# Kernel tuning notes

Measured on AMD Instinct MI355X. Metric: run time of the kernel, lower is better.

The kernel has to match this reference:

```python
import jax, jax.numpy as jnp
import numpy as np

B, N = 16, 131072
C_MID, C_OUT = 128, 16


def setup_inputs() -> dict:
    key = jax.random.key(0)
    k1, k2, k3, k4 = jax.random.split(key, 4)
    # points in roughly [-0.5, 0.5] so cube indexing covers the grids
    x = jax.random.uniform(k1, (B, N, 3), dtype=jnp.float32) - 0.5
    W1 = jax.random.normal(k2, (C_MID, 3), dtype=jnp.float32) * 0.1
    b1 = jnp.zeros((C_MID,), jnp.float32)
    W2 = jax.random.normal(k3, (C_OUT, C_MID), dtype=jnp.float32) * 0.1
    b2 = jnp.zeros((C_OUT,), jnp.float32)
    # fixed per-batch permutations (deterministic stand-in for torch.randperm)
    perm = jnp.stack([jax.random.permutation(jax.random.fold_in(k4, i), N)
                      for i in range(B)]).astype(jnp.int32)
    return {"x": x, "W1": W1, "b1": b1, "W2": W2, "b2": b2, "perm": perm}


def point_to_cell(pts, feat, W, H, D):
    # pts float [B,N,3] already clamped to [0, dim-1]; cast like torch LongTensor
    idx = pts.astype(jnp.int32)
    flat = (idx[..., 0] * H + idx[..., 1]) * D + idx[..., 2]  # [B,N]
    Bb, Nn, C = feat.shape

    def scatter_one(fi, fe):
        grid = jnp.zeros((W * H * D, C), feat.dtype)
        return grid.at[fi].set(fe)

    cell = jax.vmap(scatter_one)(flat, feat)           # [B, WHD, C]
    return cell.transpose(0, 2, 1).reshape(Bb, C, W, H, D)


def reference(x, W1, b1, W2, b2, perm):
    # PointNetfeatLocal: 1x1 Conv1d stack == per-point MLP 3 -> 128 -> 16
    h = jnp.maximum(jnp.einsum('bnc,hc->bnh', x, W1) + b1, 0.0)
    feat = jnp.einsum('bnh,oh->bno', h, W2) + b2       # [B,N,16]
    # shuffle_points_feat: per-batch permutation gather
    xs = jnp.take_along_axis(x, perm[..., None], axis=1)
    fs = jnp.take_along_axis(feat, perm[..., None], axis=1)
    # batch_grid_pooling32 / 64
    cube32 = jnp.clip(xs * 32.0 + 16.5, 0.0, 31.0)
    cube64 = jnp.clip(xs * 64.0 + 32.5, 0.0, 63.0)
    feat_cell32 = point_to_cell(cube32, fs, 32, 32, 32)  # [B,16,32,32,32]
    feat_cell64 = point_to_cell(cube64, fs, 64, 64, 64)  # [B,16,64,64,64]
    return feat_cell32, feat_cell64
```

## Files before the change

kernel.cpp:

```cpp
#include <hip/hip_runtime.h>

namespace {
constexpr int kB = 16;
constexpr int kN = 131072;
constexpr int kNLog = 17;
constexpr int kCMid = 128;
constexpr int kCOut = 16;
constexpr int kCells32Log = 15;
constexpr int kCells64Log = 18;
constexpr int kCells32 = 1 << kCells32Log;
constexpr int kCells64 = 1 << kCells64Log;
constexpr long kOut32Elems = (long)kB * kCOut * kCells32;
constexpr int kChunks32 = 16;
constexpr int kSlabs64 = 8;
constexpr int kSlabCells = kCells64 / kSlabs64;
}

typedef __bf16 bf16x8 __attribute__((ext_vector_type(8)));
typedef float f32x4 __attribute__((ext_vector_type(4)));

__device__ inline unsigned int packbf2(float lo, float hi) {
    unsigned int a = __float_as_uint(lo);
    unsigned int b = __float_as_uint(hi);
    a = (a + 0x7FFFu + ((a >> 16) & 1u)) >> 16;
    b = (b + 0x7FFFu + ((b >> 16) & 1u)) & 0xFFFF0000u;
    return b | a;
}
__device__ inline float bf_lo(unsigned int p) { return __uint_as_float(p << 16); }
__device__ inline float bf_hi(unsigned int p) { return __uint_as_float(p & 0xFFFF0000u); }

__device__ inline uint4 pack8(const float* h) {
    uint4 r;
    r.x = packbf2(h[0], h[1]); r.y = packbf2(h[2], h[3]);
    r.z = packbf2(h[4], h[5]); r.w = packbf2(h[6], h[7]);
    return r;
}

__global__ __launch_bounds__(256) void k_pack(
    const float* __restrict__ W1, const float* __restrict__ b1,
    const float* __restrict__ W2,
    float* __restrict__ W1p, uint4* __restrict__ w2h, uint4* __restrict__ w2l)
{
    const int t = threadIdx.x;
    for (int k = t; k < kCMid; k += 256) {
        W1p[k * 4 + 0] = W1[k * 3 + 0];
        W1p[k * 4 + 1] = W1[k * 3 + 1];
        W1p[k * 4 + 2] = W1[k * 3 + 2];
        W1p[k * 4 + 3] = b1[k];
    }
    {
        const int kw = t >> 6;
        const int lane = t & 63;
        const int ch = lane & 15;
        const int grp = lane >> 4;
        float v[8], lo[8];
        #pragma unroll
        for (int e = 0; e < 8; ++e)
            v[e] = W2[ch * kCMid + kw * 32 + grp * 8 + e];
        const uint4 hh = pack8(v);
        lo[0] = v[0] - bf_lo(hh.x); lo[1] = v[1] - bf_hi(hh.x);
        lo[2] = v[2] - bf_lo(hh.y); lo[3] = v[3] - bf_hi(hh.y);
        lo[4] = v[4] - bf_lo(hh.z); lo[5] = v[5] - bf_hi(hh.z);
        lo[6] = v[6] - bf_lo(hh.w); lo[7] = v[7] - bf_hi(hh.w);
        w2h[t] = hh;
        w2l[t] = pack8(lo);
    }
}

__global__ __launch_bounds__(256) void k_prep(
    const float* __restrict__ x,
    const int* __restrict__ perm,
    int* __restrict__ inv,
    unsigned int* __restrict__ cell64)
{
    const long gid = (long)blockIdx.x * 256 + threadIdx.x;
    const long bbase = gid & ~(long)(kN - 1);
    const int i = (int)(gid & (kN - 1));
    const int j = perm[gid];
    inv[bbase + j] = i;

    const float v0 = x[gid * 3 + 0];
    const float v1 = x[gid * 3 + 1];
    const float v2 = x[gid * 3 + 2];
    const int ix64 = (int)fminf(fmaxf(__fadd_rn(__fmul_rn(v0, 64.0f), 32.5f), 0.0f), 63.0f);
    const int iy64 = (int)fminf(fmaxf(__fadd_rn(__fmul_rn(v1, 64.0f), 32.5f), 0.0f), 63.0f);
    const int iz64 = (int)fminf(fmaxf(__fadd_rn(__fmul_rn(v2, 64.0f), 32.5f), 0.0f), 63.0f);
    cell64[gid] = (unsigned int)((ix64 * 64 + iy64) * 64 + iz64);
}

__global__ __launch_bounds__(256, 4) void k_mlp(
    const float* __restrict__ x,
    const float* __restrict__ W1p,
    const uint4* __restrict__ w2h, const uint4* __restrict__ w2l,
    const float* __restrict__ b2,
    uint2* __restrict__ feat)
{
    const int tid = threadIdx.x;
    const int lane = tid & 63;
    const int grp = lane >> 4;
    const int pt16 = lane & 15;
    const long base = (((long)blockIdx.x << 2) + (tid >> 6)) << 6;

    float xv[4][3];
    #pragma unroll
    for (int t = 0; t < 4; ++t) {
        const float* xp = x + (base + t * 16 + pt16) * 3;
        xv[t][0] = xp[0]; xv[t][1] = xp[1]; xv[t][2] = xp[2];
    }

    f32x4 acc[4];
    #pragma unroll
    for (int t = 0; t < 4; ++t) acc[t] = (f32x4){0.f, 0.f, 0.f, 0.f};

    const float4* __restrict__ w1v = (const float4*)W1p;

    #pragma unroll
    for (int kw = 0; kw < 4; ++kw) {
        const bf16x8 ah = __builtin_bit_cast(bf16x8, w2h[(kw << 6) + lane]);
        const bf16x8 al = __builtin_bit_cast(bf16x8, w2l[(kw << 6) + lane]);
        float4 w1r[8];
        #pragma unroll
        for (int e = 0; e < 8; ++e)
            w1r[e] = w1v[(kw << 5) + (grp << 3) + e];

        #pragma unroll
        for (int t = 0; t < 4; ++t) {
            float h[8], lo[8];
            #pragma unroll
            for (int e = 0; e < 8; ++e)
                h[e] = fmaxf(fmaf(w1r[e].x, xv[t][0],
                              fmaf(w1r[e].y, xv[t][1],
                               fmaf(w1r[e].z, xv[t][2], w1r[e].w))), 0.0f);
            const uint4 bh = pack8(h);
            lo[0] = h[0] - bf_lo(bh.x); lo[1] = h[1] - bf_hi(bh.x);
            lo[2] = h[2] - bf_lo(bh.y); lo[3] = h[3] - bf_hi(bh.y);
            lo[4] = h[4] - bf_lo(bh.z); lo[5] = h[5] - bf_hi(bh.z);
            lo[6] = h[6] - bf_lo(bh.w); lo[7] = h[7] - bf_hi(bh.w);
            const uint4 bl4 = pack8(lo);
            const bf16x8 bhv = __builtin_bit_cast(bf16x8, bh);
            const bf16x8 blv = __builtin_bit_cast(bf16x8, bl4);
            acc[t] = __builtin_amdgcn_mfma_f32_16x16x32_bf16(ah, bhv, acc[t], 0, 0, 0);
            acc[t] = __builtin_amdgcn_mfma_f32_16x16x32_bf16(ah, blv, acc[t], 0, 0, 0);
            acc[t] = __builtin_amdgcn_mfma_f32_16x16x32_bf16(al, bhv, acc[t], 0, 0, 0);
        }
    }

    const float4 bias = ((const float4*)b2)[grp];
    #pragma unroll
    for (int t = 0; t < 4; ++t) {
        const float c0 = acc[t][0] + bias.x;
        const float c1 = acc[t][1] + bias.y;
        const float c2 = acc[t][2] + bias.z;
        const float c3 = acc[t][3] + bias.w;
        uint2 o;
        o.x = packbf2(c0, c1);
        o.y = packbf2(c2, c3);
        feat[((base + t * 16 + pt16) << 2) + grp] = o;
    }
}

__global__ __launch_bounds__(1024) void k_win32(
    const float* __restrict__ x,
    const int* __restrict__ inv,
    unsigned int* __restrict__ partial32)
{
    __shared__ unsigned int lwin[kCells32];
    const int b = blockIdx.x >> 4;
    const int c = blockIdx.x & (kChunks32 - 1);
    const int t = threadIdx.x;

    #pragma unroll
    for (int r = 0; r < kCells32 / 1024; ++r) lwin[r * 1024 + t] = 0u;
    __syncthreads();

    const long base = ((long)b << kNLog) + (long)c * (kN / kChunks32);
    #pragma unroll
    for (int r = 0; r < (kN / kChunks32) / 1024; ++r) {
        const long j = base + r * 1024 + t;
        const float v0 = x[j * 3 + 0];
        const float v1 = x[j * 3 + 1];
        const float v2 = x[j * 3 + 2];
        const int ix = (int)fminf(fmaxf(__fadd_rn(__fmul_rn(v0, 32.0f), 16.5f), 0.0f), 31.0f);
        const int iy = (int)fminf(fmaxf(__fadd_rn(__fmul_rn(v1, 32.0f), 16.5f), 0.0f), 31.0f);
        const int iz = (int)fminf(fmaxf(__fadd_rn(__fmul_rn(v2, 32.0f), 16.5f), 0.0f), 31.0f);
        const unsigned int pri = (unsigned int)(inv[j] + 1);
        atomicMax(&lwin[(ix * 32 + iy) * 32 + iz], pri);
    }
    __syncthreads();

    unsigned int* dst = partial32 + ((long)blockIdx.x << kCells32Log);
    #pragma unroll
    for (int r = 0; r < kCells32 / 1024; ++r) dst[r * 1024 + t] = lwin[r * 1024 + t];
}

__global__ __launch_bounds__(1024) void k_win64(
    const unsigned int* __restrict__ cell64,
    const int* __restrict__ inv,
    unsigned int* __restrict__ win64p)
{
    __shared__ unsigned int lwin[kSlabCells];
    const int b = blockIdx.x >> 3;
    const int s = blockIdx.x & (kSlabs64 - 1);
    const int t = threadIdx.x;

    #pragma unroll
    for (int r = 0; r < kSlabCells / 1024; ++r) lwin[r * 1024 + t] = 0u;
    __syncthreads();

    const long base = (long)b << kNLog;
    for (int r = 0; r < kN / 1024; ++r) {
        const long j = base + r * 1024 + t;
        const unsigned int cell = cell64[j];
        const unsigned int pri = (unsigned int)(inv[j] + 1);
        if ((int)(cell >> 15) == s)
            atomicMax(&lwin[cell & (kSlabCells - 1)], pri);
    }
    __syncthreads();

    unsigned int* dst = win64p + ((long)b << kCells64Log) + ((long)s << 15);
    #pragma unroll
    for (int r = 0; r < kSlabCells / 1024; ++r) dst[r * 1024 + t] = lwin[r * 1024 + t];
}

__global__ __launch_bounds__(256) void k_gather32(
    const unsigned int* __restrict__ partial32,
    const int* __restrict__ perm,
    const uint4* __restrict__ feat,
    float* __restrict__ out)
{
    const long gid = (long)blockIdx.x * 256 + threadIdx.x;
    const int b = (int)(gid >> kCells32Log);
    const int cell = (int)(gid & (kCells32 - 1));

    unsigned int w = 0u;
    #pragma unroll
    for (int c = 0; c < kChunks32; ++c)
        w = max(w, partial32[(((long)(b * kChunks32 + c)) << kCells32Log) + cell]);

    float v[kCOut];
    #pragma unroll
    for (int c = 0; c < kCOut; ++c) v[c] = 0.0f;

    if (w != 0u) {
        const int i = (int)(w - 1u);
        const int j = perm[((long)b << kNLog) + i];
        const long pidx = ((long)b << kNLog) + j;
        const uint4 f0 = feat[pidx * 2 + 0];
        const uint4 f1 = feat[pidx * 2 + 1];
        v[0]  = bf_lo(f0.x); v[1]  = bf_hi(f0.x);
        v[2]  = bf_lo(f0.y); v[3]  = bf_hi(f0.y);
        v[4]  = bf_lo(f0.z); v[5]  = bf_hi(f0.z);
        v[6]  = bf_lo(f0.w); v[7]  = bf_hi(f0.w);
        v[8]  = bf_lo(f1.x); v[9]  = bf_hi(f1.x);
        v[10] = bf_lo(f1.y); v[11] = bf_hi(f1.y);
        v[12] = bf_lo(f1.z); v[13] = bf_hi(f1.z);
        v[14] = bf_lo(f1.w); v[15] = bf_hi(f1.w);
    }

    float* op = out + (((long)b * kCOut) << kCells32Log) + cell;
    #pragma unroll
    for (int c = 0; c < kCOut; ++c) op[(long)c << kCells32Log] = v[c];
}

__global__ __launch_bounds__(256) void k_gather64(
    const unsigned int* __restrict__ win,
    const int* __restrict__ perm,
    const uint4* __restrict__ feat,
    float* __restrict__ out)
{
    const long gid = (long)blockIdx.x * 256 + threadIdx.x;
    const int b = (int)(gid >> kCells64Log);
    const int cell = (int)(gid & (kCells64 - 1));
    const unsigned int w = win[gid];

    float v[kCOut];
    #pragma unroll
    for (int c = 0; c < kCOut; ++c) v[c] = 0.0f;

    if (w != 0u) {
        const int i = (int)(w - 1u);
        const int j = perm[((long)b << kNLog) + i];
        const long pidx = ((long)b << kNLog) + j;
        const uint4 f0 = feat[pidx * 2 + 0];
        const uint4 f1 = feat[pidx * 2 + 1];
        v[0]  = bf_lo(f0.x); v[1]  = bf_hi(f0.x);
        v[2]  = bf_lo(f0.y); v[3]  = bf_hi(f0.y);
        v[4]  = bf_lo(f0.z); v[5]  = bf_hi(f0.z);
        v[6]  = bf_lo(f0.w); v[7]  = bf_hi(f0.w);
        v[8]  = bf_lo(f1.x); v[9]  = bf_hi(f1.x);
        v[10] = bf_lo(f1.y); v[11] = bf_hi(f1.y);
        v[12] = bf_lo(f1.z); v[13] = bf_hi(f1.z);
        v[14] = bf_lo(f1.w); v[15] = bf_hi(f1.w);
    }

    float* op = out + (((long)b * kCOut) << kCells64Log) + cell;
    #pragma unroll
    for (int c = 0; c < kCOut; ++c) op[(long)c << kCells64Log] = v[c];
}

extern "C" void kernel_launch(void* const* d_in, const int* in_sizes, int n_in,
                              void* d_out, int out_size, void* d_ws, size_t ws_size,
                              hipStream_t stream)
{
    const float* x  = (const float*)d_in[0];
    const float* W1 = (const float*)d_in[1];
    const float* b1 = (const float*)d_in[2];
    const float* W2 = (const float*)d_in[3];
    const float* b2 = (const float*)d_in[4];
    const int* perm = (const int*)d_in[5];

    float* out32 = (float*)d_out;
    float* out64 = out32 + kOut32Elems;

    float* W1p = (float*)d_ws;
    uint4* w2h = (uint4*)((char*)d_ws + 2048);
    uint4* w2l = w2h + 256;
    int* inv = (int*)((char*)d_ws + 16384);
    unsigned int* cell64 = (unsigned int*)(inv + (size_t)kB * kN);
    unsigned int* partial32 = cell64 + (size_t)kB * kN;
    unsigned int* win64p = partial32 + (size_t)kB * kChunks32 * kCells32;
    uint4* feat = (uint4*)(win64p + (size_t)kB * kCells64);

    const int nPtsBlocks = (int)(((long)kB * kN) / 256);
    const int n32Blocks  = (int)(((long)kB * kCells32) / 256);
    const int n64Blocks  = (int)(((long)kB * kCells64) / 256);
    dim3 blk(256);

    k_pack<<<1, 256, 0, stream>>>(W1, b1, W2, W1p, w2h, w2l);
    k_prep<<<nPtsBlocks, blk, 0, stream>>>(x, perm, inv, cell64);
    k_mlp<<<nPtsBlocks, blk, 0, stream>>>(x, W1p, w2h, w2l, b2, (uint2*)feat);

    k_win32<<<kB * kChunks32, 1024, 0, stream>>>(x, inv, partial32);
    k_win64<<<kB * kSlabs64, 1024, 0, stream>>>(cell64, inv, win64p);

    k_gather32<<<n32Blocks, blk, 0, stream>>>(partial32, perm, feat, out32);
    k_gather64<<<n64Blocks, blk, 0, stream>>>(win64p, perm, feat, out64);
}
```

Baseline: 316.3 us.

## Fuse 64-grid winner selection with output gather using packed 64-bit atomics

```diff
diff --git a/kernel.cpp b/kernel.cpp
--- a/kernel.cpp
+++ b/kernel.cpp
@@ -12,7 +12,7 @@
 constexpr int kCells64 = 1 << kCells64Log;
 constexpr long kOut32Elems = (long)kB * kCOut * kCells32;
 constexpr int kChunks32 = 16;
-constexpr int kSlabs64 = 8;
+constexpr int kSlabs64 = 16;
 constexpr int kSlabCells = kCells64 / kSlabs64;
 }
 
@@ -193,33 +193,61 @@
     for (int r = 0; r < kCells32 / 1024; ++r) dst[r * 1024 + t] = lwin[r * 1024 + t];
 }
 
-__global__ __launch_bounds__(1024) void k_win64(
+__global__ __launch_bounds__(1024) void k_win64_out(
     const unsigned int* __restrict__ cell64,
     const int* __restrict__ inv,
-    unsigned int* __restrict__ win64p)
-{
-    __shared__ unsigned int lwin[kSlabCells];
-    const int b = blockIdx.x >> 3;
+    const uint4* __restrict__ feat,
+    float* __restrict__ out64)
+{
+    __shared__ unsigned long long lwin[kSlabCells];
+    const int b = blockIdx.x >> 4;
     const int s = blockIdx.x & (kSlabs64 - 1);
     const int t = threadIdx.x;
 
     #pragma unroll
-    for (int r = 0; r < kSlabCells / 1024; ++r) lwin[r * 1024 + t] = 0u;
+    for (int r = 0; r < kSlabCells / 1024; ++r) lwin[r * 1024 + t] = 0ull;
     __syncthreads();
 
     const long base = (long)b << kNLog;
     for (int r = 0; r < kN / 1024; ++r) {
-        const long j = base + r * 1024 + t;
-        const unsigned int cell = cell64[j];
-        const unsigned int pri = (unsigned int)(inv[j] + 1);
-        if ((int)(cell >> 15) == s)
-            atomicMax(&lwin[cell & (kSlabCells - 1)], pri);
+        const int j = r * 1024 + t;
+        const unsigned int cell = cell64[base + j];
+        const unsigned long long pri = (unsigned long long)(inv[base + j] + 1);
+        if ((int)(cell >> 14) == s)
+            atomicMax(&lwin[(int)(cell & (kSlabCells - 1))],
+                      (pri << 32) | (unsigned int)j);
     }
     __syncthreads();
 
-    unsigned int* dst = win64p + ((long)b << kCells64Log) + ((long)s << 15);
-    #pragma unroll
-    for (int r = 0; r < kSlabCells / 1024; ++r) dst[r * 1024 + t] = lwin[r * 1024 + t];
+    const long obase = ((long)b * kCOut) << kCells64Log;
+    #pragma unroll 2
+    for (int r = 0; r < kSlabCells / 1024; ++r) {
+        const int cl = r * 1024 + t;
+        const unsigned long long w = lwin[cl];
+
+        float v[kCOut];
+        #pragma unroll
+        for (int c = 0; c < kCOut; ++c) v[c] = 0.0f;
+
+        if (w != 0ull) {
+            const long pidx = base + (int)(w & 0xFFFFFFFFull);
+            const uint4 f0 = feat[pidx * 2 + 0];
+            const uint4 f1 = feat[pidx * 2 + 1];
+            v[0]  = bf_lo(f0.x); v[1]  = bf_hi(f0.x);
+            v[2]  = bf_lo(f0.y); v[3]  = bf_hi(f0.y);
+            v[4]  = bf_lo(f0.z); v[5]  = bf_hi(f0.z);
+            v[6]  = bf_lo(f0.w); v[7]  = bf_hi(f0.w);
+            v[8]  = bf_lo(f1.x); v[9]  = bf_hi(f1.x);
+            v[10] = bf_lo(f1.y); v[11] = bf_hi(f1.y);
+            v[12] = bf_lo(f1.z); v[13] = bf_hi(f1.z);
+            v[14] = bf_lo(f1.w); v[15] = bf_hi(f1.w);
+        }
+
+        const int cell = (s << 14) + cl;
+        float* op = out64 + obase + cell;
+        #pragma unroll
+        for (int c = 0; c < kCOut; ++c) op[(long)c << kCells64Log] = v[c];
+    }
 }
 
 __global__ __launch_bounds__(256) void k_gather32(
@@ -262,42 +290,6 @@
     for (int c = 0; c < kCOut; ++c) op[(long)c << kCells32Log] = v[c];
 }
 
-__global__ __launch_bounds__(256) void k_gather64(
-    const unsigned int* __restrict__ win,
-    const int* __restrict__ perm,
-    const uint4* __restrict__ feat,
-    float* __restrict__ out)
-{
-    const long gid = (long)blockIdx.x * 256 + threadIdx.x;
-    const int b = (int)(gid >> kCells64Log);
-    const int cell = (int)(gid & (kCells64 - 1));
-    const unsigned int w = win[gid];
-
-    float v[kCOut];
-    #pragma unroll
-    for (int c = 0; c < kCOut; ++c) v[c] = 0.0f;
-
-    if (w != 0u) {
-        const int i = (int)(w - 1u);
-        const int j = perm[((long)b << kNLog) + i];
-        const long pidx = ((long)b << kNLog) + j;
-        const uint4 f0 = feat[pidx * 2 + 0];
-        const uint4 f1 = feat[pidx * 2 + 1];
-        v[0]  = bf_lo(f0.x); v[1]  = bf_hi(f0.x);
-        v[2]  = bf_lo(f0.y); v[3]  = bf_hi(f0.y);
-        v[4]  = bf_lo(f0.z); v[5]  = bf_hi(f0.z);
-        v[6]  = bf_lo(f0.w); v[7]  = bf_hi(f0.w);
-        v[8]  = bf_lo(f1.x); v[9]  = bf_hi(f1.x);
-        v[10] = bf_lo(f1.y); v[11] = bf_hi(f1.y);
-        v[12] = bf_lo(f1.z); v[13] = bf_hi(f1.z);
-        v[14] = bf_lo(f1.w); v[15] = bf_hi(f1.w);
-    }
-
-    float* op = out + (((long)b * kCOut) << kCells64Log) + cell;
-    #pragma unroll
-    for (int c = 0; c < kCOut; ++c) op[(long)c << kCells64Log] = v[c];
-}
-
 extern "C" void kernel_launch(void* const* d_in, const int* in_sizes, int n_in,
                               void* d_out, int out_size, void* d_ws, size_t ws_size,
                               hipStream_t stream)
@@ -318,12 +310,10 @@
     int* inv = (int*)((char*)d_ws + 16384);
     unsigned int* cell64 = (unsigned int*)(inv + (size_t)kB * kN);
     unsigned int* partial32 = cell64 + (size_t)kB * kN;
-    unsigned int* win64p = partial32 + (size_t)kB * kChunks32 * kCells32;
-    uint4* feat = (uint4*)(win64p + (size_t)kB * kCells64);
+    uint4* feat = (uint4*)(partial32 + (size_t)kB * kChunks32 * kCells32);
 
     const int nPtsBlocks = (int)(((long)kB * kN) / 256);
     const int n32Blocks  = (int)(((long)kB * kCells32) / 256);
-    const int n64Blocks  = (int)(((long)kB * kCells64) / 256);
     dim3 blk(256);
 
     k_pack<<<1, 256, 0, stream>>>(W1, b1, W2, W1p, w2h, w2l);
@@ -331,8 +321,7 @@
     k_mlp<<<nPtsBlocks, blk, 0, stream>>>(x, W1p, w2h, w2l, b2, (uint2*)feat);
 
     k_win32<<<kB * kChunks32, 1024, 0, stream>>>(x, inv, partial32);
-    k_win64<<<kB * kSlabs64, 1024, 0, stream>>>(cell64, inv, win64p);
-
     k_gather32<<<n32Blocks, blk, 0, stream>>>(partial32, perm, feat, out32);
-    k_gather64<<<n64Blocks, blk, 0, stream>>>(win64p, perm, feat, out64);
-}
+
+    k_win64_out<<<kB * kSlabs64, 1024, 0, stream>>>(cell64, inv, feat, out64);
+}
```

Result: faster. 301.4 us (-4.7%).
